# Performance work log

Measured on AMD Instinct MI355X. Metric: run time of the kernel, lower is better.

Reference implementation:

```python
import jax, jax.numpy as jnp
import numpy as np

N = 4096      # num_nodes (tokens)
D = 1024      # in_features
GC1 = 1024    # gc hidden sizes
GC2 = 1024
FC1 = 512     # fc hidden
NUM_CLASSES = 2
FW = 8        # forward band width
BW = 8        # backward band width


def setup_inputs() -> dict:
    key = jax.random.key(0)
    ks = jax.random.split(key, 6)
    s = 0.02
    return {
        "x": jax.random.normal(ks[0], (N, D), jnp.float32),
        # sequential band weights, initialized to 0.5 as in the module
        "fw_w": 0.5 * jnp.ones((FW,), jnp.float32),
        "bw_w": 0.5 * jnp.ones((BW,), jnp.float32),
        # graph-conv layer weights (linear: h @ W + b, then A @ .)
        "gc_w1": s * jax.random.normal(ks[1], (D, GC1), jnp.float32),
        "gc_b1": jnp.zeros((GC1,), jnp.float32),
        "gc_w2": s * jax.random.normal(ks[2], (GC1, GC2), jnp.float32),
        "gc_b2": jnp.zeros((GC2,), jnp.float32),
        # fully-connected head
        "fc_w1": s * jax.random.normal(ks[3], (GC2, FC1), jnp.float32),
        "fc_b1": jnp.zeros((FC1,), jnp.float32),
        "fc_w2": s * jax.random.normal(ks[4], (FC1, NUM_CLASSES), jnp.float32),
        "fc_b2": jnp.zeros((NUM_CLASSES,), jnp.float32),
    }


def build_adjacency(fw_w, bw_w, n):
    # banded adjacency: self-loops + forward superdiagonals + backward subdiagonals,
    # then symmetric normalization D^{-1/2} A D^{-1/2}
    a = jnp.eye(n, dtype=fw_w.dtype)
    for j in range(fw_w.shape[0]):          # small fixed band loop (FW)
        a = a + fw_w[j] * jnp.eye(n, k=j + 1, dtype=fw_w.dtype)
    for j in range(bw_w.shape[0]):          # small fixed band loop (BW)
        a = a + bw_w[j] * jnp.eye(n, k=-(j + 1), dtype=bw_w.dtype)
    d = a.sum(axis=1) ** -0.5               # row degrees
    return d[:, None] * a * d[None, :]


def reference(x, fw_w, bw_w, gc_w1, gc_b1, gc_w2, gc_b2, fc_w1, fc_b1, fc_w2, fc_b2):
    a = build_adjacency(fw_w, bw_w, x.shape[0])          # [N, N]
    # GC layers: selu(A @ (H W + b)); dropout=0.0 -> identity
    h = jax.nn.selu(a @ (x @ gc_w1 + gc_b1))             # [N, GC1]
    h = jax.nn.selu(a @ (h @ gc_w2 + gc_b2))             # [N, GC2]
    pooled = h.mean(axis=0)                              # mean pooling over nodes
    z = jax.nn.selu(pooled @ fc_w1 + fc_b1)              # [FC1]
    return z @ fc_w2 + fc_b2                             # [NUM_CLASSES] logits
```

## Files before the change

### kernel.cpp

```cpp
#include <hip/hip_runtime.h>
#include <stdint.h>

#define NND 4096
#define DIM 1024
#define FC1N 512

typedef __attribute__((ext_vector_type(8))) short short8;
typedef __attribute__((ext_vector_type(4))) float floatx4;
typedef unsigned short u16;
typedef unsigned int u32;

__device__ inline u16 f2bf(float f) {
    union { float f; u32 u; } a; a.f = f;
    u32 u = a.u;
    u32 r = u + 0x7fffu + ((u >> 16) & 1u);
    return (u16)(r >> 16);
}
__device__ inline float bf2f(u16 h) {
    union { u32 u; float f; } a; a.u = ((u32)h) << 16; return a.f;
}
__device__ inline float selu_f(float x) {
    const float lam = 1.0507009873554805f;
    const float alp = 1.6732632423543772f;
    return x > 0.f ? lam * x : lam * alp * (expf(x) - 1.f);
}
__device__ inline void async16(const u16* g, u16* l) {
    __builtin_amdgcn_global_load_lds((const __attribute__((address_space(1))) u32*)g,
                                     (__attribute__((address_space(3))) u32*)l, 16, 0, 0);
}

__global__ void k_cvt_bf16(const float* __restrict__ in, u16* __restrict__ out) {
    int i = blockIdx.x * blockDim.x + threadIdx.x;
    float4 v = ((const float4*)in)[i];
    ushort4 o;
    o.x = f2bf(v.x); o.y = f2bf(v.y); o.z = f2bf(v.z); o.w = f2bf(v.w);
    ((ushort4*)out)[i] = o;
}

__global__ void k_transpose_cvt(const float* __restrict__ w1, const float* __restrict__ w2,
                                u16* __restrict__ o1, u16* __restrict__ o2) {
    const float* in = blockIdx.z ? w2 : w1;
    u16* out = blockIdx.z ? o2 : o1;
    __shared__ float tile[64][65];
    int r0 = blockIdx.x * 64;
    int c0 = blockIdx.y * 64;
    int t = threadIdx.x;
    int cg = t & 15, rb = t >> 4;
    #pragma unroll
    for (int rr = 0; rr < 4; ++rr) {
        int row = rb + rr * 16;
        float4 v = *(const float4*)(in + (size_t)(r0 + row) * DIM + c0 + cg * 4);
        tile[row][cg * 4 + 0] = v.x; tile[row][cg * 4 + 1] = v.y;
        tile[row][cg * 4 + 2] = v.z; tile[row][cg * 4 + 3] = v.w;
    }
    __syncthreads();
    #pragma unroll
    for (int rr = 0; rr < 4; ++rr) {
        int nl = rb + rr * 16;
        int kl = cg * 4;
        ushort4 o;
        o.x = f2bf(tile[kl + 0][nl]); o.y = f2bf(tile[kl + 1][nl]);
        o.z = f2bf(tile[kl + 2][nl]); o.w = f2bf(tile[kl + 3][nl]);
        *(ushort4*)(out + (size_t)(c0 + nl) * DIM + r0 + kl) = o;
    }
}

#define BM 128
#define BN 64
#define BK 64
__launch_bounds__(256)
__global__ void k_gemm_bf16(const u16* __restrict__ A, const u16* __restrict__ Bt,
                            const float* __restrict__ bias, u16* __restrict__ Y) {
    __shared__ u16 As[BM * BK];
    __shared__ u16 Bs[BN * BK];
    int m0 = blockIdx.x * BM, n0 = blockIdx.y * BN;
    int t = threadIdx.x, wave = t >> 6, lane = t & 63;
    int q = lane >> 4, r = lane & 15;
    int wm = wave & 1, wn = wave >> 1;
    int Lrow = lane >> 3, Lseg = lane & 7;
    floatx4 acc[4][2];
    #pragma unroll
    for (int mt = 0; mt < 4; ++mt) { acc[mt][0] = (floatx4)0.f; acc[mt][1] = (floatx4)0.f; }

    for (int k0 = 0; k0 < DIM; k0 += BK) {
        #pragma unroll
        for (int c = 0; c < 4; ++c) {
            int chunk = wave * 4 + c;
            int row = chunk * 8 + Lrow;
            const u16* g = A + (size_t)(m0 + row) * DIM + k0 + ((Lseg ^ (row & 7)) * 8);
            async16(g, &As[chunk * 8 * BK]);
        }
        #pragma unroll
        for (int c = 0; c < 2; ++c) {
            int chunk = wave * 2 + c;
            int row = chunk * 8 + Lrow;
            const u16* g = Bt + (size_t)(n0 + row) * DIM + k0 + ((Lseg ^ (row & 7)) * 8);
            async16(g, &Bs[chunk * 8 * BK]);
        }
        __syncthreads();
        #pragma unroll
        for (int s = 0; s < 2; ++s) {
            short8 bfrag[2];
            #pragma unroll
            for (int nt = 0; nt < 2; ++nt) {
                int n_loc = wn * 32 + nt * 16 + r;
                int phys = (s * 4 + q) ^ (n_loc & 7);
                bfrag[nt] = *(const short8*)&Bs[n_loc * BK + phys * 8];
            }
            #pragma unroll
            for (int mt = 0; mt < 4; ++mt) {
                int m_loc = wm * 64 + mt * 16 + r;
                int phys = (s * 4 + q) ^ (m_loc & 7);
                short8 afrag = *(const short8*)&As[m_loc * BK + phys * 8];
                acc[mt][0] = __builtin_amdgcn_mfma_f32_16x16x32_bf16(afrag, bfrag[0], acc[mt][0], 0, 0, 0);
                acc[mt][1] = __builtin_amdgcn_mfma_f32_16x16x32_bf16(afrag, bfrag[1], acc[mt][1], 0, 0, 0);
            }
        }
        __syncthreads();
    }
    #pragma unroll
    for (int nt = 0; nt < 2; ++nt) {
        int col = n0 + wn * 32 + nt * 16 + r;
        float bv = bias[col];
        #pragma unroll
        for (int mt = 0; mt < 4; ++mt)
            #pragma unroll
            for (int rr = 0; rr < 4; ++rr) {
                int row = m0 + wm * 64 + mt * 16 + q * 4 + rr;
                Y[(size_t)row * DIM + col] = f2bf(acc[mt][nt][rr] + bv);
            }
    }
}

__launch_bounds__(256)
__global__ void k_band(const u16* __restrict__ Y,
                       const float* __restrict__ fw, const float* __restrict__ bw,
                       u16* __restrict__ Hout, float* __restrict__ pooled, int mode) {
    __shared__ u16 tile[32][256];
    __shared__ float sdinv[32];
    __shared__ float wt[17];
    int i0 = blockIdx.x * 16;
    int c0 = blockIdx.y * 256;
    int t = threadIdx.x;
    if (t < 32) {
        int g = i0 - 8 + t;
        float deg = 1.f;
        #pragma unroll
        for (int j = 0; j < 8; ++j) {
            if (g + j + 1 < NND) deg += fw[j];
            if (g - j - 1 >= 0)  deg += bw[j];
        }
        sdinv[t] = (g >= 0 && g < NND) ? 1.f / sqrtf(deg) : 0.f;
    }
    if (t >= 32 && t < 49) {
        int o = t - 40;
        wt[t - 32] = (o == 0) ? 1.f : (o > 0 ? fw[o - 1] : bw[-o - 1]);
    }
    #pragma unroll
    for (int it = 0; it < 16; ++it) {
        int rl = it * 2 + (t >> 7);
        int g = i0 - 8 + rl;
        ushort2 v; v.x = 0; v.y = 0;
        if (g >= 0 && g < NND)
            v = *(const ushort2*)(Y + (size_t)g * DIM + c0 + (t & 127) * 2);
        *(ushort2*)&tile[rl][(t & 127) * 2] = v;
    }
    __syncthreads();
    float sv[32];
    #pragma unroll
    for (int rl = 0; rl < 32; ++rl) sv[rl] = sdinv[rl] * bf2f(tile[rl][t]);
    float psum = 0.f;
    #pragma unroll
    for (int rr = 0; rr < 16; ++rr) {
        float accv = 0.f;
        #pragma unroll
        for (int o = 0; o < 17; ++o) accv += wt[o] * sv[rr + o];
        float v = selu_f(accv * sdinv[rr + 8]);
        if (mode == 0) Hout[(size_t)(i0 + rr) * DIM + c0 + t] = f2bf(v);
        else psum += v;
    }
    if (mode == 1) atomicAdd(&pooled[c0 + t], psum);
}

__global__ void k_fc1(const float* __restrict__ pooled, const float* __restrict__ w1,
                      float* __restrict__ zacc) {
    int o = threadIdx.x;
    int kb = blockIdx.x * 64;
    float p = 0.f;
    for (int kk = 0; kk < 64; ++kk) {
        int k = kb + kk;
        p += pooled[k] * w1[(size_t)k * FC1N + o];
    }
    atomicAdd(&zacc[o], p * (1.f / NND));
}

__global__ void k_fc2(const float* __restrict__ zacc, const float* __restrict__ b1,
                      const float* __restrict__ w2, const float* __restrict__ b2,
                      float* __restrict__ out) {
    __shared__ float r0s[512], r1s[512];
    int o = threadIdx.x;
    float z = selu_f(zacc[o] + b1[o]);
    r0s[o] = z * w2[o * 2 + 0];
    r1s[o] = z * w2[o * 2 + 1];
    __syncthreads();
    for (int s = 256; s > 0; s >>= 1) {
        if (o < s) { r0s[o] += r0s[o + s]; r1s[o] += r1s[o + s]; }
        __syncthreads();
    }
    if (o == 0) { out[0] = r0s[0] + b2[0]; out[1] = r1s[0] + b2[1]; }
}

extern "C" void kernel_launch(void* const* d_in, const int* in_sizes, int n_in,
                              void* d_out, int out_size, void* d_ws, size_t ws_size,
                              hipStream_t stream) {
    const float* x     = (const float*)d_in[0];
    const float* fw    = (const float*)d_in[1];
    const float* bw    = (const float*)d_in[2];
    const float* gc_w1 = (const float*)d_in[3];
    const float* gc_b1 = (const float*)d_in[4];
    const float* gc_w2 = (const float*)d_in[5];
    const float* gc_b2 = (const float*)d_in[6];
    const float* fc_w1 = (const float*)d_in[7];
    const float* fc_b1 = (const float*)d_in[8];
    const float* fc_w2 = (const float*)d_in[9];
    const float* fc_b2 = (const float*)d_in[10];
    float* out = (float*)d_out;

    char* ws = (char*)d_ws;
    u16*   Xb     = (u16*)(ws + 0);
    u16*   W1t    = (u16*)(ws + (8u  << 20));
    u16*   W2t    = (u16*)(ws + (10u << 20));
    u16*   Yb     = (u16*)(ws + (12u << 20));
    float* pooled = (float*)(ws + (20u << 20));
    float* zacc   = (float*)(ws + (20u << 20) + 4096);

    hipMemsetAsync(pooled, 0, 4096 + 2048, stream);

    k_cvt_bf16<<<4096, 256, 0, stream>>>(x, Xb);
    k_transpose_cvt<<<dim3(16, 16, 2), 256, 0, stream>>>(gc_w1, gc_w2, W1t, W2t);

    k_gemm_bf16<<<dim3(32, 16), 256, 0, stream>>>(Xb, W1t, gc_b1, Yb);
    k_band<<<dim3(256, 4), 256, 0, stream>>>(Yb, fw, bw, Xb , nullptr, 0);
    k_gemm_bf16<<<dim3(32, 16), 256, 0, stream>>>(Xb , W2t, gc_b2, Yb);
    k_band<<<dim3(256, 4), 256, 0, stream>>>(Yb, fw, bw, nullptr, pooled, 1);
    k_fc1<<<16, 512, 0, stream>>>(pooled, fc_w1, zacc);
    k_fc2<<<1, 512, 0, stream>>>(zacc, fc_b1, fc_w2, fc_b2, out);
}
```

Baseline: 166.5 us.

## Fuse whole pipeline into one cooperative persistent kernel with grid syncs

Replaces the eight separate launches (memset, convert, transpose, two GEMMs, two band passes, two FC kernels) with a single cooperative kernel of 256 blocks of 512 threads, separated by grid-wide syncs. The GEMM moves to 128x128 tiles with eight waves and double-buffered async LDS loads, so the next K-slice prefetches while the current one is computed. The band stage now reads Y straight from global memory with precomputed inverse degrees instead of staging tiles in LDS. The aim is to remove launch gaps and per-kernel tails. In exchange, every stage is tied to a fixed 256-block grid and pays grid-sync cost, and the FC head stages leave most blocks idle.

```diff
diff --git a/kernel.cpp b/kernel.cpp
--- a/kernel.cpp
+++ b/kernel.cpp
@@ -1,5 +1,8 @@
 #include <hip/hip_runtime.h>
+#include <hip/hip_cooperative_groups.h>
 #include <stdint.h>
+
+namespace cg = cooperative_groups;
 
 #define NND 4096
 #define DIM 1024
@@ -10,113 +13,81 @@
 typedef unsigned short u16;
 typedef unsigned int u32;
 
-__device__ inline u16 f2bf(float f) {
+__device__ __forceinline__ u16 f2bf(float f) {
     union { float f; u32 u; } a; a.f = f;
     u32 u = a.u;
-    u32 r = u + 0x7fffu + ((u >> 16) & 1u);
-    return (u16)(r >> 16);
-}
-__device__ inline float bf2f(u16 h) {
+    return (u16)((u + 0x7fffu + ((u >> 16) & 1u)) >> 16);
+}
+__device__ __forceinline__ float bf2f(u16 h) {
     union { u32 u; float f; } a; a.u = ((u32)h) << 16; return a.f;
 }
-__device__ inline float selu_f(float x) {
+__device__ __forceinline__ float selu_f(float x) {
     const float lam = 1.0507009873554805f;
     const float alp = 1.6732632423543772f;
     return x > 0.f ? lam * x : lam * alp * (expf(x) - 1.f);
 }
-__device__ inline void async16(const u16* g, u16* l) {
+__device__ __forceinline__ void async16(const u16* g, u16* l) {
     __builtin_amdgcn_global_load_lds((const __attribute__((address_space(1))) u32*)g,
                                      (__attribute__((address_space(3))) u32*)l, 16, 0, 0);
 }
 
-__global__ void k_cvt_bf16(const float* __restrict__ in, u16* __restrict__ out) {
-    int i = blockIdx.x * blockDim.x + threadIdx.x;
-    float4 v = ((const float4*)in)[i];
-    ushort4 o;
-    o.x = f2bf(v.x); o.y = f2bf(v.y); o.z = f2bf(v.z); o.w = f2bf(v.w);
-    ((ushort4*)out)[i] = o;
-}
-
-__global__ void k_transpose_cvt(const float* __restrict__ w1, const float* __restrict__ w2,
-                                u16* __restrict__ o1, u16* __restrict__ o2) {
-    const float* in = blockIdx.z ? w2 : w1;
-    u16* out = blockIdx.z ? o2 : o1;
-    __shared__ float tile[64][65];
-    int r0 = blockIdx.x * 64;
-    int c0 = blockIdx.y * 64;
-    int t = threadIdx.x;
-    int cg = t & 15, rb = t >> 4;
-    #pragma unroll
-    for (int rr = 0; rr < 4; ++rr) {
-        int row = rb + rr * 16;
-        float4 v = *(const float4*)(in + (size_t)(r0 + row) * DIM + c0 + cg * 4);
-        tile[row][cg * 4 + 0] = v.x; tile[row][cg * 4 + 1] = v.y;
-        tile[row][cg * 4 + 2] = v.z; tile[row][cg * 4 + 3] = v.w;
-    }
-    __syncthreads();
-    #pragma unroll
-    for (int rr = 0; rr < 4; ++rr) {
-        int nl = rb + rr * 16;
-        int kl = cg * 4;
-        ushort4 o;
-        o.x = f2bf(tile[kl + 0][nl]); o.y = f2bf(tile[kl + 1][nl]);
-        o.z = f2bf(tile[kl + 2][nl]); o.w = f2bf(tile[kl + 3][nl]);
-        *(ushort4*)(out + (size_t)(c0 + nl) * DIM + r0 + kl) = o;
-    }
-}
-
-#define BM 128
-#define BN 64
-#define BK 64
-__launch_bounds__(256)
-__global__ void k_gemm_bf16(const u16* __restrict__ A, const u16* __restrict__ Bt,
-                            const float* __restrict__ bias, u16* __restrict__ Y) {
-    __shared__ u16 As[BM * BK];
-    __shared__ u16 Bs[BN * BK];
-    int m0 = blockIdx.x * BM, n0 = blockIdx.y * BN;
-    int t = threadIdx.x, wave = t >> 6, lane = t & 63;
-    int q = lane >> 4, r = lane & 15;
-    int wm = wave & 1, wn = wave >> 1;
-    int Lrow = lane >> 3, Lseg = lane & 7;
+struct P {
+    const float *x, *fw, *bw, *w1, *b1, *w2, *b2, *fcw1, *fcb1, *fcw2, *fcb2;
+    u16 *Xb, *W1t, *W2t, *Yb;
+    float *dinv, *pooled, *zacc, *out;
+};
+
+__device__ void gemm_stage(const u16* __restrict__ A, const u16* __restrict__ Bt,
+                           const float* __restrict__ bias, u16* __restrict__ Y,
+                           char* smem, int bid, int tid) {
+    const int wave = tid >> 6, lane = tid & 63;
+    const int q = lane >> 4, r = lane & 15;
+    const int wm = wave & 1, wn = wave >> 1;
+    const int Lrow = lane >> 3, Lseg = lane & 7;
+    const int m0 = (bid >> 3) * 128, n0 = (bid & 7) * 128;
+    const u16* src   = (wave < 4) ? A : Bt;
+    const int rbase  = (wave < 4) ? m0 : n0;
+    const int ldsoff = (wave < 4) ? 0 : 16384;
+    const int wv4 = wave & 3;
+
     floatx4 acc[4][2];
     #pragma unroll
     for (int mt = 0; mt < 4; ++mt) { acc[mt][0] = (floatx4)0.f; acc[mt][1] = (floatx4)0.f; }
 
-    for (int k0 = 0; k0 < DIM; k0 += BK) {
-        #pragma unroll
-        for (int c = 0; c < 4; ++c) {
-            int chunk = wave * 4 + c;
+    auto issue = [&](int b, int kb) {
+        u16* dst = (u16*)(smem + b * 32768 + ldsoff);
+        #pragma unroll
+        for (int c2 = 0; c2 < 4; ++c2) {
+            int chunk = wv4 * 4 + c2;
             int row = chunk * 8 + Lrow;
-            const u16* g = A + (size_t)(m0 + row) * DIM + k0 + ((Lseg ^ (row & 7)) * 8);
-            async16(g, &As[chunk * 8 * BK]);
-        }
-        #pragma unroll
-        for (int c = 0; c < 2; ++c) {
-            int chunk = wave * 2 + c;
-            int row = chunk * 8 + Lrow;
-            const u16* g = Bt + (size_t)(n0 + row) * DIM + k0 + ((Lseg ^ (row & 7)) * 8);
-            async16(g, &Bs[chunk * 8 * BK]);
-        }
+            async16(src + (size_t)(rbase + row) * DIM + kb + ((Lseg ^ Lrow) * 8),
+                    dst + chunk * 512);
+        }
+    };
+
+    issue(0, 0);
+    #pragma unroll 1
+    for (int k = 0; k < 16; ++k) {
         __syncthreads();
+        if (k + 1 < 16) issue((k + 1) & 1, (k + 1) * 64);
+        const u16* As = (const u16*)(smem + (k & 1) * 32768);
+        const u16* Bs = As + 8192;
         #pragma unroll
         for (int s = 0; s < 2; ++s) {
-            short8 bfrag[2];
+            short8 bfr[2];
             #pragma unroll
             for (int nt = 0; nt < 2; ++nt) {
-                int n_loc = wn * 32 + nt * 16 + r;
-                int phys = (s * 4 + q) ^ (n_loc & 7);
-                bfrag[nt] = *(const short8*)&Bs[n_loc * BK + phys * 8];
+                int nl = wn * 32 + nt * 16 + r;
+                bfr[nt] = *(const short8*)&Bs[nl * 64 + (((s * 4 + q) ^ (nl & 7)) * 8)];
             }
             #pragma unroll
             for (int mt = 0; mt < 4; ++mt) {
-                int m_loc = wm * 64 + mt * 16 + r;
-                int phys = (s * 4 + q) ^ (m_loc & 7);
-                short8 afrag = *(const short8*)&As[m_loc * BK + phys * 8];
-                acc[mt][0] = __builtin_amdgcn_mfma_f32_16x16x32_bf16(afrag, bfrag[0], acc[mt][0], 0, 0, 0);
-                acc[mt][1] = __builtin_amdgcn_mfma_f32_16x16x32_bf16(afrag, bfrag[1], acc[mt][1], 0, 0, 0);
-            }
-        }
-        __syncthreads();
+                int ml = wm * 64 + mt * 16 + r;
+                short8 afr = *(const short8*)&As[ml * 64 + (((s * 4 + q) ^ (ml & 7)) * 8)];
+                acc[mt][0] = __builtin_amdgcn_mfma_f32_16x16x32_bf16(afr, bfr[0], acc[mt][0], 0, 0, 0);
+                acc[mt][1] = __builtin_amdgcn_mfma_f32_16x16x32_bf16(afr, bfr[1], acc[mt][1], 0, 0, 0);
+            }
+        }
     }
     #pragma unroll
     for (int nt = 0; nt < 2; ++nt) {
@@ -132,117 +103,154 @@
     }
 }
 
-__launch_bounds__(256)
-__global__ void k_band(const u16* __restrict__ Y,
-                       const float* __restrict__ fw, const float* __restrict__ bw,
-                       u16* __restrict__ Hout, float* __restrict__ pooled, int mode) {
-    __shared__ u16 tile[32][256];
-    __shared__ float sdinv[32];
-    __shared__ float wt[17];
-    int i0 = blockIdx.x * 16;
-    int c0 = blockIdx.y * 256;
-    int t = threadIdx.x;
-    if (t < 32) {
-        int g = i0 - 8 + t;
-        float deg = 1.f;
-        #pragma unroll
-        for (int j = 0; j < 8; ++j) {
-            if (g + j + 1 < NND) deg += fw[j];
-            if (g - j - 1 >= 0)  deg += bw[j];
-        }
-        sdinv[t] = (g >= 0 && g < NND) ? 1.f / sqrtf(deg) : 0.f;
-    }
-    if (t >= 32 && t < 49) {
-        int o = t - 40;
-        wt[t - 32] = (o == 0) ? 1.f : (o > 0 ? fw[o - 1] : bw[-o - 1]);
-    }
+__device__ void band_stage(const u16* __restrict__ Y, const float* __restrict__ dinv,
+                           const float* __restrict__ fw, const float* __restrict__ bw,
+                           u16* __restrict__ Hout, float* __restrict__ pooled,
+                           int mode, int bid, int tid) {
+    float wt[17];
+    wt[8] = 1.f;
     #pragma unroll
-    for (int it = 0; it < 16; ++it) {
-        int rl = it * 2 + (t >> 7);
-        int g = i0 - 8 + rl;
-        ushort2 v; v.x = 0; v.y = 0;
-        if (g >= 0 && g < NND)
-            v = *(const ushort2*)(Y + (size_t)g * DIM + c0 + (t & 127) * 2);
-        *(ushort2*)&tile[rl][(t & 127) * 2] = v;
-    }
-    __syncthreads();
-    float sv[32];
-    #pragma unroll
-    for (int rl = 0; rl < 32; ++rl) sv[rl] = sdinv[rl] * bf2f(tile[rl][t]);
-    float psum = 0.f;
-    #pragma unroll
-    for (int rr = 0; rr < 16; ++rr) {
-        float accv = 0.f;
-        #pragma unroll
-        for (int o = 0; o < 17; ++o) accv += wt[o] * sv[rr + o];
-        float v = selu_f(accv * sdinv[rr + 8]);
-        if (mode == 0) Hout[(size_t)(i0 + rr) * DIM + c0 + t] = f2bf(v);
-        else psum += v;
-    }
-    if (mode == 1) atomicAdd(&pooled[c0 + t], psum);
-}
-
-__global__ void k_fc1(const float* __restrict__ pooled, const float* __restrict__ w1,
-                      float* __restrict__ zacc) {
-    int o = threadIdx.x;
-    int kb = blockIdx.x * 64;
-    float p = 0.f;
-    for (int kk = 0; kk < 64; ++kk) {
-        int k = kb + kk;
-        p += pooled[k] * w1[(size_t)k * FC1N + o];
-    }
-    atomicAdd(&zacc[o], p * (1.f / NND));
-}
-
-__global__ void k_fc2(const float* __restrict__ zacc, const float* __restrict__ b1,
-                      const float* __restrict__ w2, const float* __restrict__ b2,
-                      float* __restrict__ out) {
-    __shared__ float r0s[512], r1s[512];
-    int o = threadIdx.x;
-    float z = selu_f(zacc[o] + b1[o]);
-    r0s[o] = z * w2[o * 2 + 0];
-    r1s[o] = z * w2[o * 2 + 1];
-    __syncthreads();
-    for (int s = 256; s > 0; s >>= 1) {
-        if (o < s) { r0s[o] += r0s[o + s]; r1s[o] += r1s[o + s]; }
+    for (int j = 0; j < 8; ++j) { wt[9 + j] = fw[j]; wt[7 - j] = bw[j]; }
+    const int i0 = bid * 16;
+    #pragma unroll 1
+    for (int half = 0; half < 2; ++half) {
+        const int c = half * 512 + tid;
+        float sv[32];
+        #pragma unroll
+        for (int rl = 0; rl < 32; ++rl) {
+            int gg = i0 - 8 + rl;
+            sv[rl] = (gg >= 0 && gg < NND) ? dinv[gg] * bf2f(Y[(size_t)gg * DIM + c]) : 0.f;
+        }
+        float psum = 0.f;
+        #pragma unroll
+        for (int rr = 0; rr < 16; ++rr) {
+            float a = 0.f;
+            #pragma unroll
+            for (int o = 0; o < 17; ++o) a += wt[o] * sv[rr + o];
+            float v = selu_f(a * dinv[i0 + rr]);
+            if (mode == 0) Hout[(size_t)(i0 + rr) * DIM + c] = f2bf(v);
+            else psum += v;
+        }
+        if (mode) atomicAdd(&pooled[c], psum);
+    }
+}
+
+__global__ void __launch_bounds__(512, 2) mega(P p) {
+    cg::grid_group grid = cg::this_grid();
+    const int bid = blockIdx.x, tid = threadIdx.x;
+    __shared__ __align__(16) char smem[65536];
+
+    {
+        const float4* xin = (const float4*)p.x;
+        ushort4* xo = (ushort4*)p.Xb;
+        int base = bid * 512 + tid;
+        #pragma unroll
+        for (int i = 0; i < 8; ++i) {
+            float4 v = xin[base + i * 131072];
+            ushort4 o; o.x = f2bf(v.x); o.y = f2bf(v.y); o.z = f2bf(v.z); o.w = f2bf(v.w);
+            xo[base + i * 131072] = o;
+        }
+        if (bid == 255) {
+            for (int i = tid; i < NND; i += 512) {
+                float deg = 1.f;
+                #pragma unroll
+                for (int j = 0; j < 8; ++j) {
+                    if (i + j + 1 < NND) deg += p.fw[j];
+                    if (i - j - 1 >= 0)  deg += p.bw[j];
+                }
+                p.dinv[i] = 1.f / sqrtf(deg);
+            }
+        }
+        if (bid == 254) {
+            for (int i = tid; i < 1536; i += 512) p.pooled[i] = 0.f;
+        }
+        float (*tile)[65] = (float(*)[65])smem;
+        #pragma unroll 1
+        for (int j = 0; j < 2; ++j) {
+            int job = bid * 2 + j;
+            const float* in = (job & 256) ? p.w2 : p.w1;
+            u16* outp = (job & 256) ? p.W2t : p.W1t;
+            int tl = job & 255;
+            int r0 = (tl >> 4) * 64, c0 = (tl & 15) * 64;
+            __syncthreads();
+            {
+                int rr = tid >> 3, cs = tid & 7;
+                const float* gsrc = in + (size_t)(r0 + rr) * DIM + c0 + cs * 8;
+                float4 v0 = *(const float4*)gsrc;
+                float4 v1 = *(const float4*)(gsrc + 4);
+                float* tr = &tile[rr][cs * 8];
+                tr[0] = v0.x; tr[1] = v0.y; tr[2] = v0.z; tr[3] = v0.w;
+                tr[4] = v1.x; tr[5] = v1.y; tr[6] = v1.z; tr[7] = v1.w;
+            }
+            __syncthreads();
+            {
+                int nn = tid >> 3, ks = tid & 7;
+                union { u16 h[8]; uint4 v; } o;
+                #pragma unroll
+                for (int kk = 0; kk < 8; ++kk) o.h[kk] = f2bf(tile[ks * 8 + kk][nn]);
+                *(uint4*)(outp + (size_t)(c0 + nn) * DIM + r0 + ks * 8) = o.v;
+            }
+        }
+    }
+    grid.sync();
+    gemm_stage(p.Xb, p.W1t, p.b1, p.Yb, smem, bid, tid);
+    grid.sync();
+    band_stage(p.Yb, p.dinv, p.fw, p.bw, p.Xb , nullptr, 0, bid, tid);
+    grid.sync();
+    gemm_stage(p.Xb , p.W2t, p.b2, p.Yb, smem, bid, tid);
+    grid.sync();
+    band_stage(p.Yb, p.dinv, p.fw, p.bw, nullptr, p.pooled, 1, bid, tid);
+    grid.sync();
+    if (bid < 128) {
+        int kb = bid * 8;
+        float s = 0.f;
+        #pragma unroll
+        for (int kk = 0; kk < 8; ++kk)
+            s += p.pooled[kb + kk] * p.fcw1[(size_t)(kb + kk) * FC1N + tid];
+        atomicAdd(&p.zacc[tid], s * (1.f / NND));
+    }
+    grid.sync();
+    if (bid == 0) {
+        float* red = (float*)smem;
+        float z = selu_f(p.zacc[tid] + p.fcb1[tid]);
+        red[tid] = z * p.fcw2[tid * 2 + 0];
+        red[512 + tid] = z * p.fcw2[tid * 2 + 1];
         __syncthreads();
-    }
-    if (o == 0) { out[0] = r0s[0] + b2[0]; out[1] = r1s[0] + b2[1]; }
+        #pragma unroll 1
+        for (int s2 = 256; s2 > 0; s2 >>= 1) {
+            if (tid < s2) { red[tid] += red[tid + s2]; red[512 + tid] += red[512 + tid + s2]; }
+            __syncthreads();
+        }
+        if (tid == 0) { p.out[0] = red[0] + p.fcb2[0]; p.out[1] = red[1] + p.fcb2[1]; }
+    }
 }
 
 extern "C" void kernel_launch(void* const* d_in, const int* in_sizes, int n_in,
                               void* d_out, int out_size, void* d_ws, size_t ws_size,
                               hipStream_t stream) {
-    const float* x     = (const float*)d_in[0];
-    const float* fw    = (const float*)d_in[1];
-    const float* bw    = (const float*)d_in[2];
-    const float* gc_w1 = (const float*)d_in[3];
-    const float* gc_b1 = (const float*)d_in[4];
-    const float* gc_w2 = (const float*)d_in[5];
-    const float* gc_b2 = (const float*)d_in[6];
-    const float* fc_w1 = (const float*)d_in[7];
-    const float* fc_b1 = (const float*)d_in[8];
-    const float* fc_w2 = (const float*)d_in[9];
-    const float* fc_b2 = (const float*)d_in[10];
-    float* out = (float*)d_out;
-
     char* ws = (char*)d_ws;
-    u16*   Xb     = (u16*)(ws + 0);
-    u16*   W1t    = (u16*)(ws + (8u  << 20));
-    u16*   W2t    = (u16*)(ws + (10u << 20));
-    u16*   Yb     = (u16*)(ws + (12u << 20));
-    float* pooled = (float*)(ws + (20u << 20));
-    float* zacc   = (float*)(ws + (20u << 20) + 4096);
-
-    hipMemsetAsync(pooled, 0, 4096 + 2048, stream);
-
-    k_cvt_bf16<<<4096, 256, 0, stream>>>(x, Xb);
-    k_transpose_cvt<<<dim3(16, 16, 2), 256, 0, stream>>>(gc_w1, gc_w2, W1t, W2t);
-
-    k_gemm_bf16<<<dim3(32, 16), 256, 0, stream>>>(Xb, W1t, gc_b1, Yb);
-    k_band<<<dim3(256, 4), 256, 0, stream>>>(Yb, fw, bw, Xb , nullptr, 0);
-    k_gemm_bf16<<<dim3(32, 16), 256, 0, stream>>>(Xb , W2t, gc_b2, Yb);
-    k_band<<<dim3(256, 4), 256, 0, stream>>>(Yb, fw, bw, nullptr, pooled, 1);
-    k_fc1<<<16, 512, 0, stream>>>(pooled, fc_w1, zacc);
-    k_fc2<<<1, 512, 0, stream>>>(zacc, fc_b1, fc_w2, fc_b2, out);
-}
+    P p;
+    p.x    = (const float*)d_in[0];
+    p.fw   = (const float*)d_in[1];
+    p.bw   = (const float*)d_in[2];
+    p.w1   = (const float*)d_in[3];
+    p.b1   = (const float*)d_in[4];
+    p.w2   = (const float*)d_in[5];
+    p.b2   = (const float*)d_in[6];
+    p.fcw1 = (const float*)d_in[7];
+    p.fcb1 = (const float*)d_in[8];
+    p.fcw2 = (const float*)d_in[9];
+    p.fcb2 = (const float*)d_in[10];
+    p.Xb   = (u16*)(ws);
+    p.W1t  = (u16*)(ws + (8u  << 20));
+    p.W2t  = (u16*)(ws + (10u << 20));
+    p.Yb   = (u16*)(ws + (12u << 20));
+    p.dinv = (float*)(ws + (20u << 20));
+    p.pooled = (float*)(ws + (20u << 20) + 16384);
+    p.zacc = p.pooled + 1024;
+    p.out  = (float*)d_out;
+
+    void* args[] = { &p };
+    hipLaunchCooperativeKernel(reinterpret_cast<void*>(mega), dim3(256), dim3(512),
+                               args, 0, stream);
+}
```

Measured after the change: 414.9 us. 149% more time.
